# Optimization experiments

Measured on AMD Instinct MI355X. Metric: run time of the kernel, lower is better.

Reference implementation:

```python
import jax, jax.numpy as jnp
import numpy as np

WIN_LEN = 5
RES_LEN = None


def _log_sparse_mask(Q_L, K_L, win_len=0, res_len=None):
    # Faithful port of LogSparseMask (numpy, static shapes -> constant-folded under jit)
    if res_len is None:
        L_ls = K_L - 1 - win_len
        n_reps = 1
    else:
        n_reps = int(np.ceil(K_L / res_len))
        L_ls = res_len
    l_floor = int(np.log2(L_ls))
    indxs = np.array([int(2 ** (l_floor - i)) for i in range(l_floor + 1)])
    reps_array = np.expand_dims(np.arange(n_reps, dtype='int') * L_ls, 1)
    indxs = (indxs + reps_array + win_len).flatten()
    indxs = indxs[indxs < K_L - 1]
    my_mask = np.ones(K_L, dtype='int')
    my_mask[indxs] = 0
    my_mask[:win_len + 1] = 0
    my_mask = np.concatenate([np.flip(my_mask[1:]), my_mask])
    my_mask = np.array([my_mask[K_L - i:K_L * 2 - i] for i in range(1, Q_L + 1)], dtype=bool)
    return my_mask  # [Q_L, K_L], True = masked out


def _combined_mask(L, S):
    causal = np.triu(np.ones((L, S), dtype=bool), k=1)  # TriangularCausalMask
    sparse = _log_sparse_mask(L, S, WIN_LEN, RES_LEN)
    return jnp.asarray(causal | sparse)[None, None]  # [1,1,L,S], broadcasts over B,H


def setup_inputs() -> dict:
    key = jax.random.key(0)
    k1, k2, k3 = jax.random.split(key, 3)
    B, L, H, E, D = 4, 2048, 8, 64, 64
    return {
        'queries': jax.random.normal(k1, (B, L, H, E), dtype=jnp.float32),
        'keys': jax.random.normal(k2, (B, L, H, E), dtype=jnp.float32),
        'values': jax.random.normal(k3, (B, L, H, D), dtype=jnp.float32),
    }


def reference(queries, keys, values):
    B, L, H, E = queries.shape
    S = keys.shape[1]
    scale = 1.0 / np.sqrt(E)  # self.scale is None -> 1/sqrt(E)
    # [B,H,L,S] full score matrix (eager), then causal|log-sparse masked_fill(-inf)
    scores = jnp.einsum('blhe,bshe->bhls', queries, keys)
    mask = _combined_mask(L, S)
    scores = jnp.where(mask, -jnp.inf, scale * scores)
    A = jax.nn.softmax(scores, axis=-1)  # dropout p=0.0 (eval) -> identity
    V = jnp.einsum('bhls,bshd->blhd', A, values)
    return V  # module returns (V, None); attention weights not output
```

## Files before the change

### kernel.cpp

```cpp
#include <hip/hip_runtime.h>
#include <stdint.h>


static constexpr int Bn = 4, Ln = 2048, Hn = 8, En = 64;
static constexpr int NDELTA = 17;
static constexpr int NEAR_MAX = 37;
static constexpr int SPAN = 69;
static constexpr int PADF = 68;

__global__ __launch_bounds__(256) void logsparse_attn_kernel(
    const float* __restrict__ Q,
    const float* __restrict__ K,
    const float* __restrict__ V,
    float* __restrict__ O)
{
    constexpr int deltas[NDELTA] = {0,1,2,3,4,5,6,7,9,13,21,37,69,133,261,517,1029};

    __shared__ float Ks[SPAN * PADF];
    __shared__ float Vs[SPAN * PADF];

    const int bh = blockIdx.x & 31;
    const int l  = blockIdx.x >> 5;
    const int b  = bh >> 3;
    const int h  = bh & 7;
    const int q0 = l * 32;

    const int tid = threadIdx.x;
    const size_t bhBase = ((size_t)b * Ln * Hn + (size_t)h) * (size_t)En;
    constexpr int ROWF = Hn * En;

    for (int idx = tid; idx < 2 * SPAN * 16; idx += 256) {
        const int ten = (idx >= SPAN * 16);
        const int rem = ten ? idx - SPAN * 16 : idx;
        const int rid = rem >> 4;
        const int ch  = rem & 15;
        int g = q0 - NEAR_MAX + rid;
        if (g < 0) g = 0;
        const float* src = (ten ? V : K) + bhBase + (size_t)g * ROWF + ch * 4;
        float* dst = (ten ? Vs : Ks) + rid * PADF + ch * 4;
        *(float4*)dst = *(const float4*)src;
    }
    __syncthreads();

    const int sub = tid & 7;
    const int qq  = tid >> 3;
    const int q   = q0 + qq;
    const int dimOff = sub * 8;
    const size_t rowQ = bhBase + (size_t)q * ROWF;

    const float4 q0v = *(const float4*)(Q + rowQ + dimOff);
    const float4 q1v = *(const float4*)(Q + rowQ + dimOff + 4);
    const float qf[8] = { q0v.x*0.125f, q0v.y*0.125f, q0v.z*0.125f, q0v.w*0.125f,
                          q1v.x*0.125f, q1v.y*0.125f, q1v.z*0.125f, q1v.w*0.125f };

    float sc[NDELTA];
    #pragma unroll
    for (int d = 0; d < NDELTA; ++d) {
        const int del = deltas[d];
        const int j   = q - del;
        float4 k0, k1;
        if (del <= NEAR_MAX) {
            const float* kp = Ks + (qq + NEAR_MAX - del) * PADF + dimOff;
            k0 = *(const float4*)(kp);
            k1 = *(const float4*)(kp + 4);
        } else {
            const int jc = (j < 0) ? 0 : j;
            const float* kp = K + bhBase + (size_t)jc * ROWF + dimOff;
            k0 = *(const float4*)(kp);
            k1 = *(const float4*)(kp + 4);
        }
        float s = qf[0]*k0.x + qf[1]*k0.y + qf[2]*k0.z + qf[3]*k0.w
                + qf[4]*k1.x + qf[5]*k1.y + qf[6]*k1.z + qf[7]*k1.w;
        s += __shfl_xor(s, 1);
        s += __shfl_xor(s, 2);
        s += __shfl_xor(s, 4);
        sc[d] = (j < 0) ? -__builtin_inff() : s;
    }

    float m = sc[0];
    #pragma unroll
    for (int d = 1; d < NDELTA; ++d) m = fmaxf(m, sc[d]);
    float p[NDELTA];
    float sum = 0.0f;
    #pragma unroll
    for (int d = 0; d < NDELTA; ++d) {
        p[d] = __expf(sc[d] - m);
        sum += p[d];
    }
    const float inv = 1.0f / sum;

    float acc[8] = {0,0,0,0,0,0,0,0};
    #pragma unroll
    for (int d = 0; d < NDELTA; ++d) {
        const int del = deltas[d];
        const int j   = q - del;
        float4 v0, v1;
        if (del <= NEAR_MAX) {
            const float* vp = Vs + (qq + NEAR_MAX - del) * PADF + dimOff;
            v0 = *(const float4*)(vp);
            v1 = *(const float4*)(vp + 4);
        } else {
            const int jc = (j < 0) ? 0 : j;
            const float* vp = V + bhBase + (size_t)jc * ROWF + dimOff;
            v0 = *(const float4*)(vp);
            v1 = *(const float4*)(vp + 4);
        }
        const float w = p[d];
        acc[0] = fmaf(w, v0.x, acc[0]);
        acc[1] = fmaf(w, v0.y, acc[1]);
        acc[2] = fmaf(w, v0.z, acc[2]);
        acc[3] = fmaf(w, v0.w, acc[3]);
        acc[4] = fmaf(w, v1.x, acc[4]);
        acc[5] = fmaf(w, v1.y, acc[5]);
        acc[6] = fmaf(w, v1.z, acc[6]);
        acc[7] = fmaf(w, v1.w, acc[7]);
    }

    float4 o0, o1;
    o0.x = acc[0]*inv; o0.y = acc[1]*inv; o0.z = acc[2]*inv; o0.w = acc[3]*inv;
    o1.x = acc[4]*inv; o1.y = acc[5]*inv; o1.z = acc[6]*inv; o1.w = acc[7]*inv;
    *(float4*)(O + rowQ + dimOff)     = o0;
    *(float4*)(O + rowQ + dimOff + 4) = o1;
}

extern "C" void kernel_launch(void* const* d_in, const int* in_sizes, int n_in,
                              void* d_out, int out_size, void* d_ws, size_t ws_size,
                              hipStream_t stream) {
    const float* Q = (const float*)d_in[0];
    const float* K = (const float*)d_in[1];
    const float* V = (const float*)d_in[2];
    float* O = (float*)d_out;

    const int nblocks = Bn * Hn * (Ln / 32);
    logsparse_attn_kernel<<<nblocks, 256, 0, stream>>>(Q, K, V, O);
}
```

Measured before the change: 102.6 us.

## Enlarge query tile, stage more near keys in LDS, prefetch far K/V early

Each block now handles 64 queries with 512 threads, and the shared-memory window widens so deltas up to 69 come from LDS. The Q load and the far-offset K loads are issued before the barrier so they overlap the K/V staging copy. Far V loads are issued before the softmax. Whole far deltas are skipped for blocks where they are entirely causal-masked. This raises register pressure and doubles LDS per block, which may limit occupancy.

```diff
diff --git a/kernel.cpp b/kernel.cpp
--- a/kernel.cpp
+++ b/kernel.cpp
@@ -3,18 +3,23 @@
 
 
 static constexpr int Bn = 4, Ln = 2048, Hn = 8, En = 64;
-static constexpr int NDELTA = 17;
-static constexpr int NEAR_MAX = 37;
-static constexpr int SPAN = 69;
+static constexpr int QPB = 64;
+static constexpr int NT  = 512;
+static constexpr int NEAR_MAX = 69;
+static constexpr int SPAN = NEAR_MAX + QPB;
 static constexpr int PADF = 68;
+static constexpr int NNEAR = 13;
+static constexpr int NFAR  = 4;
+static constexpr int NDELTA = NNEAR + NFAR;
 
-__global__ __launch_bounds__(256) void logsparse_attn_kernel(
+__global__ __launch_bounds__(NT, 4) void logsparse_attn_kernel(
     const float* __restrict__ Q,
     const float* __restrict__ K,
     const float* __restrict__ V,
     float* __restrict__ O)
 {
-    constexpr int deltas[NDELTA] = {0,1,2,3,4,5,6,7,9,13,21,37,69,133,261,517,1029};
+    constexpr int nearD[NNEAR] = {0,1,2,3,4,5,6,7,9,13,21,37,69};
+    constexpr int farD[NFAR]   = {133,261,517,1029};
 
     __shared__ float Ks[SPAN * PADF];
     __shared__ float Vs[SPAN * PADF];
@@ -23,58 +28,92 @@
     const int l  = blockIdx.x >> 5;
     const int b  = bh >> 3;
     const int h  = bh & 7;
-    const int q0 = l * 32;
+    const int q0 = l * QPB;
 
     const int tid = threadIdx.x;
     const size_t bhBase = ((size_t)b * Ln * Hn + (size_t)h) * (size_t)En;
     constexpr int ROWF = Hn * En;
 
-    for (int idx = tid; idx < 2 * SPAN * 16; idx += 256) {
-        const int ten = (idx >= SPAN * 16);
-        const int rem = ten ? idx - SPAN * 16 : idx;
-        const int rid = rem >> 4;
-        const int ch  = rem & 15;
-        int g = q0 - NEAR_MAX + rid;
-        if (g < 0) g = 0;
-        const float* src = (ten ? V : K) + bhBase + (size_t)g * ROWF + ch * 4;
-        float* dst = (ten ? Vs : Ks) + rid * PADF + ch * 4;
-        *(float4*)dst = *(const float4*)src;
-    }
-    __syncthreads();
-
     const int sub = tid & 7;
     const int qq  = tid >> 3;
     const int q   = q0 + qq;
     const int dimOff = sub * 8;
-    const size_t rowQ = bhBase + (size_t)q * ROWF;
+    const size_t rowQ = bhBase + (size_t)q * ROWF + dimOff;
 
-    const float4 q0v = *(const float4*)(Q + rowQ + dimOff);
-    const float4 q1v = *(const float4*)(Q + rowQ + dimOff + 4);
+    const float4 q0v = *(const float4*)(Q + rowQ);
+    const float4 q1v = *(const float4*)(Q + rowQ + 4);
+
+    for (int idx = tid; idx < SPAN * 16; idx += NT) {
+        const int rid = idx >> 4;
+        const int ch  = idx & 15;
+        int g = q0 - NEAR_MAX + rid;
+        if (g < 0) g = 0;
+        const size_t srcOff = bhBase + (size_t)g * ROWF + ch * 4;
+        const int dst = rid * PADF + ch * 4;
+        *(float4*)(Ks + dst) = *(const float4*)(K + srcOff);
+        *(float4*)(Vs + dst) = *(const float4*)(V + srcOff);
+    }
+
     const float qf[8] = { q0v.x*0.125f, q0v.y*0.125f, q0v.z*0.125f, q0v.w*0.125f,
                           q1v.x*0.125f, q1v.y*0.125f, q1v.z*0.125f, q1v.w*0.125f };
 
+    bool farOn[NFAR];
+    float4 fk0[NFAR], fk1[NFAR];
+    #pragma unroll
+    for (int d = 0; d < NFAR; ++d) {
+        const int del = farD[d];
+        farOn[d] = (q0 + QPB - 1 >= del);
+        if (farOn[d]) {
+            const int j  = q - del;
+            const int jc = (j < 0) ? 0 : j;
+            const float* kp = K + bhBase + (size_t)jc * ROWF + dimOff;
+            fk0[d] = *(const float4*)(kp);
+            fk1[d] = *(const float4*)(kp + 4);
+        }
+    }
+
+    __syncthreads();
+
     float sc[NDELTA];
     #pragma unroll
-    for (int d = 0; d < NDELTA; ++d) {
-        const int del = deltas[d];
-        const int j   = q - del;
-        float4 k0, k1;
-        if (del <= NEAR_MAX) {
-            const float* kp = Ks + (qq + NEAR_MAX - del) * PADF + dimOff;
-            k0 = *(const float4*)(kp);
-            k1 = *(const float4*)(kp + 4);
-        } else {
-            const int jc = (j < 0) ? 0 : j;
-            const float* kp = K + bhBase + (size_t)jc * ROWF + dimOff;
-            k0 = *(const float4*)(kp);
-            k1 = *(const float4*)(kp + 4);
-        }
+    for (int d = 0; d < NNEAR; ++d) {
+        const int del = nearD[d];
+        const float* kp = Ks + (qq + NEAR_MAX - del) * PADF + dimOff;
+        const float4 k0 = *(const float4*)(kp);
+        const float4 k1 = *(const float4*)(kp + 4);
         float s = qf[0]*k0.x + qf[1]*k0.y + qf[2]*k0.z + qf[3]*k0.w
                 + qf[4]*k1.x + qf[5]*k1.y + qf[6]*k1.z + qf[7]*k1.w;
         s += __shfl_xor(s, 1);
         s += __shfl_xor(s, 2);
         s += __shfl_xor(s, 4);
-        sc[d] = (j < 0) ? -__builtin_inff() : s;
+        sc[d] = (q - del < 0) ? -__builtin_inff() : s;
+    }
+
+    #pragma unroll
+    for (int d = 0; d < NFAR; ++d) {
+        const int del = farD[d];
+        float s = -__builtin_inff();
+        if (farOn[d]) {
+            float t = qf[0]*fk0[d].x + qf[1]*fk0[d].y + qf[2]*fk0[d].z + qf[3]*fk0[d].w
+                    + qf[4]*fk1[d].x + qf[5]*fk1[d].y + qf[6]*fk1[d].z + qf[7]*fk1[d].w;
+            t += __shfl_xor(t, 1);
+            t += __shfl_xor(t, 2);
+            t += __shfl_xor(t, 4);
+            s = (q - del < 0) ? -__builtin_inff() : t;
+        }
+        sc[NNEAR + d] = s;
+    }
+
+    float4 fv0[NFAR], fv1[NFAR];
+    #pragma unroll
+    for (int d = 0; d < NFAR; ++d) {
+        if (farOn[d]) {
+            const int j  = q - farD[d];
+            const int jc = (j < 0) ? 0 : j;
+            const float* vp = V + bhBase + (size_t)jc * ROWF + dimOff;
+            fv0[d] = *(const float4*)(vp);
+            fv1[d] = *(const float4*)(vp + 4);
+        }
     }
 
     float m = sc[0];
@@ -91,20 +130,11 @@
 
     float acc[8] = {0,0,0,0,0,0,0,0};
     #pragma unroll
-    for (int d = 0; d < NDELTA; ++d) {
-        const int del = deltas[d];
-        const int j   = q - del;
-        float4 v0, v1;
-        if (del <= NEAR_MAX) {
-            const float* vp = Vs + (qq + NEAR_MAX - del) * PADF + dimOff;
-            v0 = *(const float4*)(vp);
-            v1 = *(const float4*)(vp + 4);
-        } else {
-            const int jc = (j < 0) ? 0 : j;
-            const float* vp = V + bhBase + (size_t)jc * ROWF + dimOff;
-            v0 = *(const float4*)(vp);
-            v1 = *(const float4*)(vp + 4);
-        }
+    for (int d = 0; d < NNEAR; ++d) {
+        const int del = nearD[d];
+        const float* vp = Vs + (qq + NEAR_MAX - del) * PADF + dimOff;
+        const float4 v0 = *(const float4*)(vp);
+        const float4 v1 = *(const float4*)(vp + 4);
         const float w = p[d];
         acc[0] = fmaf(w, v0.x, acc[0]);
         acc[1] = fmaf(w, v0.y, acc[1]);
@@ -115,12 +145,26 @@
         acc[6] = fmaf(w, v1.z, acc[6]);
         acc[7] = fmaf(w, v1.w, acc[7]);
     }
+    #pragma unroll
+    for (int d = 0; d < NFAR; ++d) {
+        if (farOn[d]) {
+            const float w = p[NNEAR + d];
+            acc[0] = fmaf(w, fv0[d].x, acc[0]);
+            acc[1] = fmaf(w, fv0[d].y, acc[1]);
+            acc[2] = fmaf(w, fv0[d].z, acc[2]);
+            acc[3] = fmaf(w, fv0[d].w, acc[3]);
+            acc[4] = fmaf(w, fv1[d].x, acc[4]);
+            acc[5] = fmaf(w, fv1[d].y, acc[5]);
+            acc[6] = fmaf(w, fv1[d].z, acc[6]);
+            acc[7] = fmaf(w, fv1[d].w, acc[7]);
+        }
+    }
 
     float4 o0, o1;
     o0.x = acc[0]*inv; o0.y = acc[1]*inv; o0.z = acc[2]*inv; o0.w = acc[3]*inv;
     o1.x = acc[4]*inv; o1.y = acc[5]*inv; o1.z = acc[6]*inv; o1.w = acc[7]*inv;
-    *(float4*)(O + rowQ + dimOff)     = o0;
-    *(float4*)(O + rowQ + dimOff + 4) = o1;
+    *(float4*)(O + rowQ)     = o0;
+    *(float4*)(O + rowQ + 4) = o1;
 }
 
 extern "C" void kernel_launch(void* const* d_in, const int* in_sizes, int n_in,
@@ -131,6 +175,6 @@
     const float* V = (const float*)d_in[2];
     float* O = (float*)d_out;
 
-    const int nblocks = Bn * Hn * (Ln / 32);
-    logsparse_attn_kernel<<<nblocks, 256, 0, stream>>>(Q, K, V, O);
+    const int nblocks = Bn * Hn * (Ln / QPB);
+    logsparse_attn_kernel<<<nblocks, NT, 0, stream>>>(Q, K, V, O);
 }
```

After: 128.1 us. 1.25x slower.

## Drop shared-memory K/V staging and load all keys/values directly from global

Applied to the files above, without the earlier changes.

Removes the shared-memory tile of nearby K/V rows and the block barrier, so each thread issues all 17 K and 17 V float4 loads straight from global memory, with loads batched ahead of use. The mapping becomes 16 threads per query with 4 dims each and 16 queries per block, doubling the block count. This trades the redundant staging of 69 rows per 32 queries for reliance on L1/L2 caching of overlapping near rows. It also raises register pressure from holding 34 float4 values.

```diff
diff --git a/kernel.cpp b/kernel.cpp
--- a/kernel.cpp
+++ b/kernel.cpp
@@ -3,124 +3,88 @@
 
 
 static constexpr int Bn = 4, Ln = 2048, Hn = 8, En = 64;
-static constexpr int NDELTA = 17;
-static constexpr int NEAR_MAX = 37;
-static constexpr int SPAN = 69;
-static constexpr int PADF = 68;
+static constexpr int QPB = 16;
+static constexpr int NT  = 256;
+static constexpr int ND  = 17;
 
-__global__ __launch_bounds__(256) void logsparse_attn_kernel(
+__global__ __launch_bounds__(NT) void logsparse_attn_kernel(
     const float* __restrict__ Q,
     const float* __restrict__ K,
     const float* __restrict__ V,
     float* __restrict__ O)
 {
-    constexpr int deltas[NDELTA] = {0,1,2,3,4,5,6,7,9,13,21,37,69,133,261,517,1029};
-
-    __shared__ float Ks[SPAN * PADF];
-    __shared__ float Vs[SPAN * PADF];
+    constexpr int deltas[ND] = {0,1,2,3,4,5,6,7,9,13,21,37,69,133,261,517,1029};
 
     const int bh = blockIdx.x & 31;
     const int l  = blockIdx.x >> 5;
     const int b  = bh >> 3;
     const int h  = bh & 7;
-    const int q0 = l * 32;
+    const int q0 = l * QPB;
 
     const int tid = threadIdx.x;
     const size_t bhBase = ((size_t)b * Ln * Hn + (size_t)h) * (size_t)En;
     constexpr int ROWF = Hn * En;
 
-    for (int idx = tid; idx < 2 * SPAN * 16; idx += 256) {
-        const int ten = (idx >= SPAN * 16);
-        const int rem = ten ? idx - SPAN * 16 : idx;
-        const int rid = rem >> 4;
-        const int ch  = rem & 15;
-        int g = q0 - NEAR_MAX + rid;
-        if (g < 0) g = 0;
-        const float* src = (ten ? V : K) + bhBase + (size_t)g * ROWF + ch * 4;
-        float* dst = (ten ? Vs : Ks) + rid * PADF + ch * 4;
-        *(float4*)dst = *(const float4*)src;
+    const int sub = tid & 15;
+    const int qq  = tid >> 4;
+    const int q   = q0 + qq;
+    const int dimOff = sub * 4;
+    const size_t rowQ = bhBase + (size_t)q * ROWF + dimOff;
+
+    const float4 qv = *(const float4*)(Q + rowQ);
+    const float qf[4] = { qv.x*0.125f, qv.y*0.125f, qv.z*0.125f, qv.w*0.125f };
+
+    float4 k[ND];
+    #pragma unroll
+    for (int d = 0; d < ND; ++d) {
+        const int j  = q - deltas[d];
+        const int jc = (j < 0) ? 0 : j;
+        k[d] = *(const float4*)(K + bhBase + (size_t)jc * ROWF + dimOff);
     }
-    __syncthreads();
 
-    const int sub = tid & 7;
-    const int qq  = tid >> 3;
-    const int q   = q0 + qq;
-    const int dimOff = sub * 8;
-    const size_t rowQ = bhBase + (size_t)q * ROWF;
-
-    const float4 q0v = *(const float4*)(Q + rowQ + dimOff);
-    const float4 q1v = *(const float4*)(Q + rowQ + dimOff + 4);
-    const float qf[8] = { q0v.x*0.125f, q0v.y*0.125f, q0v.z*0.125f, q0v.w*0.125f,
-                          q1v.x*0.125f, q1v.y*0.125f, q1v.z*0.125f, q1v.w*0.125f };
-
-    float sc[NDELTA];
+    float sc[ND];
     #pragma unroll
-    for (int d = 0; d < NDELTA; ++d) {
-        const int del = deltas[d];
-        const int j   = q - del;
-        float4 k0, k1;
-        if (del <= NEAR_MAX) {
-            const float* kp = Ks + (qq + NEAR_MAX - del) * PADF + dimOff;
-            k0 = *(const float4*)(kp);
-            k1 = *(const float4*)(kp + 4);
-        } else {
-            const int jc = (j < 0) ? 0 : j;
-            const float* kp = K + bhBase + (size_t)jc * ROWF + dimOff;
-            k0 = *(const float4*)(kp);
-            k1 = *(const float4*)(kp + 4);
-        }
-        float s = qf[0]*k0.x + qf[1]*k0.y + qf[2]*k0.z + qf[3]*k0.w
-                + qf[4]*k1.x + qf[5]*k1.y + qf[6]*k1.z + qf[7]*k1.w;
+    for (int d = 0; d < ND; ++d) {
+        float s = qf[0]*k[d].x + qf[1]*k[d].y + qf[2]*k[d].z + qf[3]*k[d].w;
         s += __shfl_xor(s, 1);
         s += __shfl_xor(s, 2);
         s += __shfl_xor(s, 4);
-        sc[d] = (j < 0) ? -__builtin_inff() : s;
+        s += __shfl_xor(s, 8);
+        sc[d] = (q - deltas[d] < 0) ? -__builtin_inff() : s;
+    }
+
+    float4 v[ND];
+    #pragma unroll
+    for (int d = 0; d < ND; ++d) {
+        const int j  = q - deltas[d];
+        const int jc = (j < 0) ? 0 : j;
+        v[d] = *(const float4*)(V + bhBase + (size_t)jc * ROWF + dimOff);
     }
 
     float m = sc[0];
     #pragma unroll
-    for (int d = 1; d < NDELTA; ++d) m = fmaxf(m, sc[d]);
-    float p[NDELTA];
+    for (int d = 1; d < ND; ++d) m = fmaxf(m, sc[d]);
     float sum = 0.0f;
     #pragma unroll
-    for (int d = 0; d < NDELTA; ++d) {
-        p[d] = __expf(sc[d] - m);
-        sum += p[d];
+    for (int d = 0; d < ND; ++d) {
+        sc[d] = __expf(sc[d] - m);
+        sum += sc[d];
     }
     const float inv = 1.0f / sum;
 
-    float acc[8] = {0,0,0,0,0,0,0,0};
+    float acc[4] = {0,0,0,0};
     #pragma unroll
-    for (int d = 0; d < NDELTA; ++d) {
-        const int del = deltas[d];
-        const int j   = q - del;
-        float4 v0, v1;
-        if (del <= NEAR_MAX) {
-            const float* vp = Vs + (qq + NEAR_MAX - del) * PADF + dimOff;
-            v0 = *(const float4*)(vp);
-            v1 = *(const float4*)(vp + 4);
-        } else {
-            const int jc = (j < 0) ? 0 : j;
-            const float* vp = V + bhBase + (size_t)jc * ROWF + dimOff;
-            v0 = *(const float4*)(vp);
-            v1 = *(const float4*)(vp + 4);
-        }
-        const float w = p[d];
-        acc[0] = fmaf(w, v0.x, acc[0]);
-        acc[1] = fmaf(w, v0.y, acc[1]);
-        acc[2] = fmaf(w, v0.z, acc[2]);
-        acc[3] = fmaf(w, v0.w, acc[3]);
-        acc[4] = fmaf(w, v1.x, acc[4]);
-        acc[5] = fmaf(w, v1.y, acc[5]);
-        acc[6] = fmaf(w, v1.z, acc[6]);
-        acc[7] = fmaf(w, v1.w, acc[7]);
+    for (int d = 0; d < ND; ++d) {
+        const float w = sc[d];
+        acc[0] = fmaf(w, v[d].x, acc[0]);
+        acc[1] = fmaf(w, v[d].y, acc[1]);
+        acc[2] = fmaf(w, v[d].z, acc[2]);
+        acc[3] = fmaf(w, v[d].w, acc[3]);
     }
 
-    float4 o0, o1;
-    o0.x = acc[0]*inv; o0.y = acc[1]*inv; o0.z = acc[2]*inv; o0.w = acc[3]*inv;
-    o1.x = acc[4]*inv; o1.y = acc[5]*inv; o1.z = acc[6]*inv; o1.w = acc[7]*inv;
-    *(float4*)(O + rowQ + dimOff)     = o0;
-    *(float4*)(O + rowQ + dimOff + 4) = o1;
+    float4 o;
+    o.x = acc[0]*inv; o.y = acc[1]*inv; o.z = acc[2]*inv; o.w = acc[3]*inv;
+    *(float4*)(O + rowQ) = o;
 }
 
 extern "C" void kernel_launch(void* const* d_in, const int* in_sizes, int n_in,
@@ -131,6 +95,6 @@
     const float* V = (const float*)d_in[2];
     float* O = (float*)d_out;
 
-    const int nblocks = Bn * Hn * (Ln / 32);
-    logsparse_attn_kernel<<<nblocks, 256, 0, stream>>>(Q, K, V, O);
+    const int nblocks = Bn * Hn * (Ln / QPB);
+    logsparse_attn_kernel<<<nblocks, NT, 0, stream>>>(Q, K, V, O);
 }
```

Measured after the change: 103.6 us. Within noise of the previous version (+1.0%).
